# Optimization experiments

Hardware: AMD Instinct MI355X
Metric: run time of the kernel (lower is better)

The kernel has to match this reference:

```python
import jax, jax.numpy as jnp
import numpy as np

L, A, S, D, H = 64, 64, 20, 512, 8
HD = D // H  # head_dim = 64


def _linear(x, W, b):
    # torch nn.Linear: y = x @ W.T + b, W is [out, in]
    return x @ W.T + b


def _mha(q, k, v, mask, Wq, bq, Wk, bk, Wv, bv, Wo, bo):
    # q,k,v: [L, B, D]; mask: [Lq, Lk] additive float mask
    Lq, B, Dm = q.shape
    Lk = k.shape[0]
    scale = 1.0 / np.sqrt(HD)
    qh = _linear(q, Wq, bq).reshape(Lq, B, H, HD) * scale
    kh = _linear(k, Wk, bk).reshape(Lk, B, H, HD)
    vh = _linear(v, Wv, bv).reshape(Lk, B, H, HD)
    scores = jnp.einsum('qbhd,kbhd->bhqk', qh, kh) + mask[None, None, :, :]
    p = jax.nn.softmax(scores, axis=-1)
    o = jnp.einsum('bhqk,kbhd->qbhd', p, vh).reshape(Lq, B, Dm)
    return _linear(o, Wo, bo)


def _forward(query, key, value, attn_mask, Wq, bq, Wk, bk, Wv, bv, Wo, bo,
             Wti, bti, Wtg, btg, seq_mask):
    Lq, Ag, Sm, Dm = query.shape
    Lk = key.shape[0]
    B = Ag * Sm
    # temporal causal mask (torch loop: rows i mask cols > i; built only if seq_mask and Lq==Lk)
    if seq_mask and Lq == Lk:
        tmask = jnp.where(jnp.arange(Lq)[:, None] < jnp.arange(Lk)[None, :],
                          -jnp.inf, 0.0).astype(query.dtype)
    else:
        tmask = jnp.zeros((Lq, Lk), dtype=query.dtype)
    tq = query.reshape(Lq, B, Dm)
    tk = key.reshape(Lk, B, Dm)
    tv = value.reshape(Lk, B, Dm)
    t_attn = _mha(tq, tk, tv, tmask, Wq, bq, Wk, bk, Wv, bv, Wo, bo)
    # GLU-style gated fusion
    t_out = jnp.tanh(_linear(t_attn, Wti, bti)) * jax.nn.sigmoid(_linear(t_attn, Wtg, btg))
    return t_out.reshape(Lq, Ag, Sm, Dm)


def setup_inputs() -> dict:
    key = jax.random.key(0)
    ks = jax.random.split(key, 16)
    sd = 1.0 / np.sqrt(D)
    f32 = jnp.float32
    inp = {
        'query': jax.random.normal(ks[0], (L, A, S, D), f32),
        'key': jax.random.normal(ks[1], (L, A, S, D), f32),
        'value': jax.random.normal(ks[2], (L, A, S, D), f32),
        'attn_mask': jnp.zeros((L, L), f32),
        'Wq': jax.random.normal(ks[3], (D, D), f32) * sd,
        'bq': jnp.zeros((D,), f32),
        'Wk': jax.random.normal(ks[4], (D, D), f32) * sd,
        'bk': jnp.zeros((D,), f32),
        'Wv': jax.random.normal(ks[5], (D, D), f32) * sd,
        'bv': jnp.zeros((D,), f32),
        'Wo': jax.random.normal(ks[6], (D, D), f32) * sd,
        'bo': jnp.zeros((D,), f32),
        'Wti': jax.random.normal(ks[7], (D, D), f32) * sd,
        'bti': jnp.zeros((D,), f32),
        'Wtg': jax.random.normal(ks[8], (D, D), f32) * sd,
        'btg': jnp.zeros((D,), f32),
        'seq_mask': 1,
    }
    return inp


def reference(query, key, value, attn_mask, Wq, bq, Wk, bk, Wv, bv, Wo, bo,
              Wti, bti, Wtg, btg, seq_mask):
    return _forward(query, key, value, attn_mask, Wq, bq, Wk, bk, Wv, bv,
                    Wo, bo, Wti, bti, Wtg, btg, seq_mask)
```

## Files before the change

### kernel.cpp

```cpp
#include <hip/hip_runtime.h>
#include <hip/hip_bf16.h>
#include <math.h>
#include <stdint.h>

typedef __hip_bfloat16 bf16_t;
typedef __bf16 bf16x8 __attribute__((ext_vector_type(8)));
typedef float f32x4 __attribute__((ext_vector_type(4)));

#define MFMA_BF16(a, b, c) __builtin_amdgcn_mfma_f32_16x16x32_bf16((a), (b), (c), 0, 0, 0)

__device__ __forceinline__ uint4 ld8_f32_bf16(const float* p) {
  const float4 x = *(const float4*)p;
  const float4 y = *(const float4*)(p + 4);
  union { bf16_t h[8]; uint4 u; } r;
  r.h[0] = __float2bfloat16(x.x); r.h[1] = __float2bfloat16(x.y);
  r.h[2] = __float2bfloat16(x.z); r.h[3] = __float2bfloat16(x.w);
  r.h[4] = __float2bfloat16(y.x); r.h[5] = __float2bfloat16(y.y);
  r.h[6] = __float2bfloat16(y.z); r.h[7] = __float2bfloat16(y.w);
  return r.u;
}

__global__ __launch_bounds__(256) void gemm_f32(const float* __restrict__ A,
                                                const float* __restrict__ W,
                                                const float* __restrict__ bias,
                                                bf16_t* __restrict__ C, float alpha) {
  const int K = 512, N = 512;
  __shared__ __align__(16) bf16_t As[128 * 32];
  __shared__ __align__(16) bf16_t Bs[128 * 32];
  const int tid = threadIdx.x;
  const int w = tid >> 6, lane = tid & 63;
  const int quad = lane >> 4, l16 = lane & 15;
  const int wm = (w >> 1) * 64, wn = (w & 1) * 64;
  const size_t m0 = (size_t)blockIdx.x * 128;
  const int n0 = blockIdx.y * 128;
  const float* Ab = A + m0 * K;
  const float* Wb = W + (size_t)n0 * K;
  const int r0 = tid >> 2;
  const int c0 = (tid & 3) * 8;
  f32x4 acc[4][4] = {};
  for (int k0 = 0; k0 < K; k0 += 32) {
    const uint4 a0 = ld8_f32_bf16(&Ab[(size_t)r0 * K + k0 + c0]);
    const uint4 a1 = ld8_f32_bf16(&Ab[(size_t)(r0 + 64) * K + k0 + c0]);
    const uint4 b0 = ld8_f32_bf16(&Wb[(size_t)r0 * K + k0 + c0]);
    const uint4 b1 = ld8_f32_bf16(&Wb[(size_t)(r0 + 64) * K + k0 + c0]);
    __syncthreads();
    *(uint4*)&As[r0 * 32 + c0] = a0;
    *(uint4*)&As[(r0 + 64) * 32 + c0] = a1;
    *(uint4*)&Bs[r0 * 32 + c0] = b0;
    *(uint4*)&Bs[(r0 + 64) * 32 + c0] = b1;
    __syncthreads();
    bf16x8 af[4], bfr[4];
#pragma unroll
    for (int i = 0; i < 4; i++)
      af[i] = *(const bf16x8*)&As[(wm + i * 16 + l16) * 32 + quad * 8];
#pragma unroll
    for (int j = 0; j < 4; j++)
      bfr[j] = *(const bf16x8*)&Bs[(wn + j * 16 + l16) * 32 + quad * 8];
#pragma unroll
    for (int i = 0; i < 4; i++)
#pragma unroll
      for (int j = 0; j < 4; j++)
        acc[i][j] = MFMA_BF16(af[i], bfr[j], acc[i][j]);
  }
#pragma unroll
  for (int j = 0; j < 4; j++) {
    const int col = n0 + wn + j * 16 + l16;
    const float bv = bias[col];
#pragma unroll
    for (int i = 0; i < 4; i++) {
      const size_t row = m0 + wm + i * 16 + quad * 4;
#pragma unroll
      for (int v = 0; v < 4; v++) {
        const float x = (acc[i][j][v] + bv) * alpha;
        C[(row + v) * N + col] = __float2bfloat16(x);
      }
    }
  }
}

__global__ __launch_bounds__(256) void gemm_abf16(const bf16_t* __restrict__ A,
                                                  const float* __restrict__ W,
                                                  const float* __restrict__ bias,
                                                  bf16_t* __restrict__ C) {
  const int K = 512, N = 512;
  __shared__ __align__(16) bf16_t As[128 * 32];
  __shared__ __align__(16) bf16_t Bs[128 * 32];
  const int tid = threadIdx.x;
  const int w = tid >> 6, lane = tid & 63;
  const int quad = lane >> 4, l16 = lane & 15;
  const int wm = (w >> 1) * 64, wn = (w & 1) * 64;
  const size_t m0 = (size_t)blockIdx.x * 128;
  const int n0 = blockIdx.y * 128;
  const bf16_t* Ab = A + m0 * K;
  const float* Wb = W + (size_t)n0 * K;
  const int r0 = tid >> 2;
  const int c0 = (tid & 3) * 8;
  f32x4 acc[4][4] = {};
  for (int k0 = 0; k0 < K; k0 += 32) {
    const uint4 a0 = *(const uint4*)&Ab[(size_t)r0 * K + k0 + c0];
    const uint4 a1 = *(const uint4*)&Ab[(size_t)(r0 + 64) * K + k0 + c0];
    const uint4 b0 = ld8_f32_bf16(&Wb[(size_t)r0 * K + k0 + c0]);
    const uint4 b1 = ld8_f32_bf16(&Wb[(size_t)(r0 + 64) * K + k0 + c0]);
    __syncthreads();
    *(uint4*)&As[r0 * 32 + c0] = a0;
    *(uint4*)&As[(r0 + 64) * 32 + c0] = a1;
    *(uint4*)&Bs[r0 * 32 + c0] = b0;
    *(uint4*)&Bs[(r0 + 64) * 32 + c0] = b1;
    __syncthreads();
    bf16x8 af[4], bfr[4];
#pragma unroll
    for (int i = 0; i < 4; i++)
      af[i] = *(const bf16x8*)&As[(wm + i * 16 + l16) * 32 + quad * 8];
#pragma unroll
    for (int j = 0; j < 4; j++)
      bfr[j] = *(const bf16x8*)&Bs[(wn + j * 16 + l16) * 32 + quad * 8];
#pragma unroll
    for (int i = 0; i < 4; i++)
#pragma unroll
      for (int j = 0; j < 4; j++)
        acc[i][j] = MFMA_BF16(af[i], bfr[j], acc[i][j]);
  }
#pragma unroll
  for (int j = 0; j < 4; j++) {
    const int col = n0 + wn + j * 16 + l16;
    const float bv = bias[col];
#pragma unroll
    for (int i = 0; i < 4; i++) {
      const size_t row = m0 + wm + i * 16 + quad * 4;
#pragma unroll
      for (int v = 0; v < 4; v++) {
        const float x = acc[i][j][v] + bv;
        C[(row + v) * N + col] = __float2bfloat16(x);
      }
    }
  }
}

__global__ __launch_bounds__(256) void gemm_gate(const bf16_t* __restrict__ A,
                                                 const float* __restrict__ Wi,
                                                 const float* __restrict__ bi,
                                                 const float* __restrict__ Wg,
                                                 const float* __restrict__ bg,
                                                 float* __restrict__ C) {
  const int K = 512, N = 512;
  __shared__ __align__(16) bf16_t As[128 * 32];
  __shared__ __align__(16) bf16_t Bi[128 * 32];
  __shared__ __align__(16) bf16_t Bg[128 * 32];
  const int tid = threadIdx.x;
  const int w = tid >> 6, lane = tid & 63;
  const int quad = lane >> 4, l16 = lane & 15;
  const int wm = (w >> 1) * 64, wn = (w & 1) * 64;
  const size_t m0 = (size_t)blockIdx.x * 128;
  const int n0 = blockIdx.y * 128;
  const bf16_t* Ab = A + m0 * K;
  const float* Wib = Wi + (size_t)n0 * K;
  const float* Wgb = Wg + (size_t)n0 * K;
  const int r0 = tid >> 2;
  const int c0 = (tid & 3) * 8;
  f32x4 ai[4][4] = {};
  f32x4 ag[4][4] = {};
  for (int k0 = 0; k0 < K; k0 += 32) {
    const uint4 a0 = *(const uint4*)&Ab[(size_t)r0 * K + k0 + c0];
    const uint4 a1 = *(const uint4*)&Ab[(size_t)(r0 + 64) * K + k0 + c0];
    const uint4 i0 = ld8_f32_bf16(&Wib[(size_t)r0 * K + k0 + c0]);
    const uint4 i1 = ld8_f32_bf16(&Wib[(size_t)(r0 + 64) * K + k0 + c0]);
    const uint4 g0 = ld8_f32_bf16(&Wgb[(size_t)r0 * K + k0 + c0]);
    const uint4 g1 = ld8_f32_bf16(&Wgb[(size_t)(r0 + 64) * K + k0 + c0]);
    __syncthreads();
    *(uint4*)&As[r0 * 32 + c0] = a0;
    *(uint4*)&As[(r0 + 64) * 32 + c0] = a1;
    *(uint4*)&Bi[r0 * 32 + c0] = i0;
    *(uint4*)&Bi[(r0 + 64) * 32 + c0] = i1;
    *(uint4*)&Bg[r0 * 32 + c0] = g0;
    *(uint4*)&Bg[(r0 + 64) * 32 + c0] = g1;
    __syncthreads();
    bf16x8 af[4], bif[4], bgf[4];
#pragma unroll
    for (int i = 0; i < 4; i++)
      af[i] = *(const bf16x8*)&As[(wm + i * 16 + l16) * 32 + quad * 8];
#pragma unroll
    for (int j = 0; j < 4; j++) {
      bif[j] = *(const bf16x8*)&Bi[(wn + j * 16 + l16) * 32 + quad * 8];
      bgf[j] = *(const bf16x8*)&Bg[(wn + j * 16 + l16) * 32 + quad * 8];
    }
#pragma unroll
    for (int i = 0; i < 4; i++)
#pragma unroll
      for (int j = 0; j < 4; j++) {
        ai[i][j] = MFMA_BF16(af[i], bif[j], ai[i][j]);
        ag[i][j] = MFMA_BF16(af[i], bgf[j], ag[i][j]);
      }
  }
#pragma unroll
  for (int j = 0; j < 4; j++) {
    const int col = n0 + wn + j * 16 + l16;
    const float bvi = bi[col];
    const float bvg = bg[col];
#pragma unroll
    for (int i = 0; i < 4; i++) {
      const size_t row = m0 + wm + i * 16 + quad * 4;
#pragma unroll
      for (int v = 0; v < 4; v++) {
        const float xi = ai[i][j][v] + bvi;
        const float xg = ag[i][j][v] + bvg;
        C[(row + v) * N + col] = tanhf(xi) * (1.0f / (1.0f + __expf(-xg)));
      }
    }
  }
}

__global__ __launch_bounds__(64) void attn_head(const bf16_t* Qh,
                                                const bf16_t* Kh,
                                                const bf16_t* Vh,
                                                bf16_t* O,
                                                const int* __restrict__ seq_mask) {
  const int B = 1280, D = 512;
  const int b = blockIdx.x >> 3, h = blockIdx.x & 7;
  const int lane = threadIdx.x;
  __shared__ __align__(16) bf16_t Qs[64 * 64];
  __shared__ __align__(16) bf16_t Ks[64 * 64];
  __shared__ __align__(16) bf16_t VT[64 * 64];
  bf16_t* Ps = Qs;
  const size_t cb = (size_t)h * 64;
  for (int idx = lane; idx < 512; idx += 64) {
    const int r = idx >> 3, cg = (idx & 7) << 3;
    const size_t go = (size_t)(r * B + b) * D + cb + cg;
    *(uint4*)&Qs[r * 64 + cg] = *(const uint4*)&Qh[go];
    *(uint4*)&Ks[r * 64 + cg] = *(const uint4*)&Kh[go];
    uint4 vv = *(const uint4*)&Vh[go];
    const bf16_t* vp = (const bf16_t*)&vv;
#pragma unroll
    for (int jj = 0; jj < 8; jj++) VT[(cg + jj) * 64 + r] = vp[jj];
  }
  __syncthreads();
  const int quad = lane >> 4, l16 = lane & 15;
  f32x4 sc[4][4] = {};
#pragma unroll
  for (int ks = 0; ks < 2; ks++) {
    bf16x8 qa[4], kb[4];
#pragma unroll
    for (int i = 0; i < 4; i++)
      qa[i] = *(const bf16x8*)&Qs[(i * 16 + l16) * 64 + ks * 32 + quad * 8];
#pragma unroll
    for (int j = 0; j < 4; j++)
      kb[j] = *(const bf16x8*)&Ks[(j * 16 + l16) * 64 + ks * 32 + quad * 8];
#pragma unroll
    for (int i = 0; i < 4; i++)
#pragma unroll
      for (int j = 0; j < 4; j++)
        sc[i][j] = MFMA_BF16(qa[i], kb[j], sc[i][j]);
  }
  const bool causal = (seq_mask[0] != 0);
  __syncthreads();
#pragma unroll
  for (int i = 0; i < 4; i++) {
#pragma unroll
    for (int v = 0; v < 4; v++) {
      const int r = i * 16 + quad * 4 + v;
      float sv[4];
      float mx = -3e38f;
#pragma unroll
      for (int j = 0; j < 4; j++) {
        const int c = j * 16 + l16;
        float s = sc[i][j][v];
        if (causal && c > r) s = -3e38f;
        sv[j] = s;
        mx = fmaxf(mx, s);
      }
#pragma unroll
      for (int m = 1; m < 16; m <<= 1) mx = fmaxf(mx, __shfl_xor(mx, m, 16));
      float sum = 0.f;
#pragma unroll
      for (int j = 0; j < 4; j++) {
        const float e = (sv[j] <= -1e38f) ? 0.f : __expf(sv[j] - mx);
        sv[j] = e;
        sum += e;
      }
#pragma unroll
      for (int m = 1; m < 16; m <<= 1) sum += __shfl_xor(sum, m, 16);
      const float inv = 1.0f / sum;
#pragma unroll
      for (int j = 0; j < 4; j++)
        Ps[r * 64 + j * 16 + l16] = __float2bfloat16(sv[j] * inv);
    }
  }
  __syncthreads();
  f32x4 oc[4][4] = {};
#pragma unroll
  for (int ks = 0; ks < 2; ks++) {
    bf16x8 pf[4], vf[4];
#pragma unroll
    for (int i = 0; i < 4; i++)
      pf[i] = *(const bf16x8*)&Ps[(i * 16 + l16) * 64 + ks * 32 + quad * 8];
#pragma unroll
    for (int j = 0; j < 4; j++)
      vf[j] = *(const bf16x8*)&VT[(j * 16 + l16) * 64 + ks * 32 + quad * 8];
#pragma unroll
    for (int i = 0; i < 4; i++)
#pragma unroll
      for (int j = 0; j < 4; j++)
        oc[i][j] = MFMA_BF16(pf[i], vf[j], oc[i][j]);
  }
#pragma unroll
  for (int i = 0; i < 4; i++)
#pragma unroll
    for (int j = 0; j < 4; j++) {
      const int c = j * 16 + l16;
#pragma unroll
      for (int v = 0; v < 4; v++) {
        const int r = i * 16 + quad * 4 + v;
        O[(size_t)(r * B + b) * D + cb + c] = __float2bfloat16(oc[i][j][v]);
      }
    }
}

extern "C" void kernel_launch(void* const* d_in, const int* in_sizes, int n_in,
                              void* d_out, int out_size, void* d_ws, size_t ws_size,
                              hipStream_t stream) {
  const float* query = (const float*)d_in[0];
  const float* key_ = (const float*)d_in[1];
  const float* value = (const float*)d_in[2];
  const float* Wq = (const float*)d_in[4];
  const float* bq = (const float*)d_in[5];
  const float* Wk = (const float*)d_in[6];
  const float* bk = (const float*)d_in[7];
  const float* Wv = (const float*)d_in[8];
  const float* bv = (const float*)d_in[9];
  const float* Wo = (const float*)d_in[10];
  const float* bo = (const float*)d_in[11];
  const float* Wti = (const float*)d_in[12];
  const float* bti = (const float*)d_in[13];
  const float* Wtg = (const float*)d_in[14];
  const float* btg = (const float*)d_in[15];
  const int* seq_mask = (const int*)d_in[16];
  float* out = (float*)d_out;

  const size_t M = 81920;
  const size_t buf = M * 512;
  bf16_t* Qh = (bf16_t*)d_ws;
  bf16_t* Kh = Qh + buf;
  bf16_t* Vh = Kh + buf;
  bf16_t* Ob = Qh;
  bf16_t* Ta = Kh;

  dim3 gg(640, 4), gb(256);
  hipLaunchKernelGGL(gemm_f32, gg, gb, 0, stream, query, Wq, bq, Qh, 0.125f);
  hipLaunchKernelGGL(gemm_f32, gg, gb, 0, stream, key_, Wk, bk, Kh, 1.0f);
  hipLaunchKernelGGL(gemm_f32, gg, gb, 0, stream, value, Wv, bv, Vh, 1.0f);
  hipLaunchKernelGGL(attn_head, dim3(10240), dim3(64), 0, stream, Qh, Kh, Vh, Ob, seq_mask);
  hipLaunchKernelGGL(gemm_abf16, gg, gb, 0, stream, Ob, Wo, bo, Ta);
  hipLaunchKernelGGL(gemm_gate, gg, gb, 0, stream, Ta, Wti, bti, Wtg, btg, out);
}
```

Baseline: 1.311 ms.

## Pre-convert weights to bf16 and stage GEMM tiles via direct global-to-LDS loads

A new kernel converts all six fp32 weight matrices to bf16 once per call into extra workspace. This removes the per-block fp32-to-bf16 conversion and halves weight read traffic in every GEMM tile. The bf16 operand tiles are now copied with global_load_lds straight into shared memory, skipping the register round-trip. The fp32-input projection GEMM also prefetches the next A tile into registers before the MFMA loop. The cost is one extra small launch and more workspace, and correctness relies on the LDS DMA lane layout and on completion before the barrier.

```diff
diff --git a/kernel.cpp b/kernel.cpp
--- a/kernel.cpp
+++ b/kernel.cpp
@@ -20,10 +20,43 @@
   return r.u;
 }
 
-__global__ __launch_bounds__(256) void gemm_f32(const float* __restrict__ A,
-                                                const float* __restrict__ W,
-                                                const float* __restrict__ bias,
-                                                bf16_t* __restrict__ C, float alpha) {
+__device__ __forceinline__ uint4 pack8_bf16(const float4 x, const float4 y) {
+  union { bf16_t h[8]; uint4 u; } r;
+  r.h[0] = __float2bfloat16(x.x); r.h[1] = __float2bfloat16(x.y);
+  r.h[2] = __float2bfloat16(x.z); r.h[3] = __float2bfloat16(x.w);
+  r.h[4] = __float2bfloat16(y.x); r.h[5] = __float2bfloat16(y.y);
+  r.h[6] = __float2bfloat16(y.z); r.h[7] = __float2bfloat16(y.w);
+  return r.u;
+}
+
+__device__ __forceinline__ void gload16(const bf16_t* g, bf16_t* lds) {
+  __builtin_amdgcn_global_load_lds(
+      (const __attribute__((address_space(1))) void*)g,
+      (__attribute__((address_space(3))) void*)lds, 16, 0, 0);
+}
+
+__global__ __launch_bounds__(256) void cvt_w6(const float* __restrict__ W0,
+                                              const float* __restrict__ W1,
+                                              const float* __restrict__ W2,
+                                              const float* __restrict__ W3,
+                                              const float* __restrict__ W4,
+                                              const float* __restrict__ W5,
+                                              bf16_t* __restrict__ dst) {
+  const int m = blockIdx.y;
+  const float* src = W0;
+  if (m == 1) src = W1;
+  else if (m == 2) src = W2;
+  else if (m == 3) src = W3;
+  else if (m == 4) src = W4;
+  else if (m == 5) src = W5;
+  const size_t i = ((size_t)blockIdx.x * 256 + threadIdx.x) * 8;
+  *(uint4*)&dst[(size_t)m * 262144 + i] = ld8_f32_bf16(&src[i]);
+}
+
+__global__ __launch_bounds__(256) void gemm_aw(const float* __restrict__ A,
+                                               const bf16_t* __restrict__ W,
+                                               const float* __restrict__ bias,
+                                               bf16_t* __restrict__ C, float alpha) {
   const int K = 512, N = 512;
   __shared__ __align__(16) bf16_t As[128 * 32];
   __shared__ __align__(16) bf16_t Bs[128 * 32];
@@ -34,20 +67,22 @@
   const size_t m0 = (size_t)blockIdx.x * 128;
   const int n0 = blockIdx.y * 128;
   const float* Ab = A + m0 * K;
-  const float* Wb = W + (size_t)n0 * K;
+  const bf16_t* Wb = W + (size_t)n0 * K;
   const int r0 = tid >> 2;
   const int c0 = (tid & 3) * 8;
   f32x4 acc[4][4] = {};
+  float4 pa0 = *(const float4*)&Ab[(size_t)r0 * K + c0];
+  float4 pa1 = *(const float4*)&Ab[(size_t)r0 * K + c0 + 4];
+  float4 pa2 = *(const float4*)&Ab[(size_t)(r0 + 64) * K + c0];
+  float4 pa3 = *(const float4*)&Ab[(size_t)(r0 + 64) * K + c0 + 4];
   for (int k0 = 0; k0 < K; k0 += 32) {
-    const uint4 a0 = ld8_f32_bf16(&Ab[(size_t)r0 * K + k0 + c0]);
-    const uint4 a1 = ld8_f32_bf16(&Ab[(size_t)(r0 + 64) * K + k0 + c0]);
-    const uint4 b0 = ld8_f32_bf16(&Wb[(size_t)r0 * K + k0 + c0]);
-    const uint4 b1 = ld8_f32_bf16(&Wb[(size_t)(r0 + 64) * K + k0 + c0]);
-    __syncthreads();
+    const uint4 a0 = pack8_bf16(pa0, pa1);
+    const uint4 a1 = pack8_bf16(pa2, pa3);
+    __syncthreads();
+    gload16(&Wb[(size_t)r0 * K + k0 + c0], &Bs[w * 512]);
+    gload16(&Wb[(size_t)(r0 + 64) * K + k0 + c0], &Bs[2048 + w * 512]);
     *(uint4*)&As[r0 * 32 + c0] = a0;
     *(uint4*)&As[(r0 + 64) * 32 + c0] = a1;
-    *(uint4*)&Bs[r0 * 32 + c0] = b0;
-    *(uint4*)&Bs[(r0 + 64) * 32 + c0] = b1;
     __syncthreads();
     bf16x8 af[4], bfr[4];
 #pragma unroll
@@ -56,6 +91,12 @@
 #pragma unroll
     for (int j = 0; j < 4; j++)
       bfr[j] = *(const bf16x8*)&Bs[(wn + j * 16 + l16) * 32 + quad * 8];
+    if (k0 + 32 < K) {
+      pa0 = *(const float4*)&Ab[(size_t)r0 * K + k0 + 32 + c0];
+      pa1 = *(const float4*)&Ab[(size_t)r0 * K + k0 + 32 + c0 + 4];
+      pa2 = *(const float4*)&Ab[(size_t)(r0 + 64) * K + k0 + 32 + c0];
+      pa3 = *(const float4*)&Ab[(size_t)(r0 + 64) * K + k0 + 32 + c0 + 4];
+    }
 #pragma unroll
     for (int i = 0; i < 4; i++)
 #pragma unroll
@@ -78,10 +119,10 @@
   }
 }
 
-__global__ __launch_bounds__(256) void gemm_abf16(const bf16_t* __restrict__ A,
-                                                  const float* __restrict__ W,
-                                                  const float* __restrict__ bias,
-                                                  bf16_t* __restrict__ C) {
+__global__ __launch_bounds__(256) void gemm_bb(const bf16_t* __restrict__ A,
+                                               const bf16_t* __restrict__ W,
+                                               const float* __restrict__ bias,
+                                               bf16_t* __restrict__ C) {
   const int K = 512, N = 512;
   __shared__ __align__(16) bf16_t As[128 * 32];
   __shared__ __align__(16) bf16_t Bs[128 * 32];
@@ -92,20 +133,16 @@
   const size_t m0 = (size_t)blockIdx.x * 128;
   const int n0 = blockIdx.y * 128;
   const bf16_t* Ab = A + m0 * K;
-  const float* Wb = W + (size_t)n0 * K;
+  const bf16_t* Wb = W + (size_t)n0 * K;
   const int r0 = tid >> 2;
   const int c0 = (tid & 3) * 8;
   f32x4 acc[4][4] = {};
   for (int k0 = 0; k0 < K; k0 += 32) {
-    const uint4 a0 = *(const uint4*)&Ab[(size_t)r0 * K + k0 + c0];
-    const uint4 a1 = *(const uint4*)&Ab[(size_t)(r0 + 64) * K + k0 + c0];
-    const uint4 b0 = ld8_f32_bf16(&Wb[(size_t)r0 * K + k0 + c0]);
-    const uint4 b1 = ld8_f32_bf16(&Wb[(size_t)(r0 + 64) * K + k0 + c0]);
-    __syncthreads();
-    *(uint4*)&As[r0 * 32 + c0] = a0;
-    *(uint4*)&As[(r0 + 64) * 32 + c0] = a1;
-    *(uint4*)&Bs[r0 * 32 + c0] = b0;
-    *(uint4*)&Bs[(r0 + 64) * 32 + c0] = b1;
+    __syncthreads();
+    gload16(&Ab[(size_t)r0 * K + k0 + c0], &As[w * 512]);
+    gload16(&Ab[(size_t)(r0 + 64) * K + k0 + c0], &As[2048 + w * 512]);
+    gload16(&Wb[(size_t)r0 * K + k0 + c0], &Bs[w * 512]);
+    gload16(&Wb[(size_t)(r0 + 64) * K + k0 + c0], &Bs[2048 + w * 512]);
     __syncthreads();
     bf16x8 af[4], bfr[4];
 #pragma unroll
@@ -136,12 +173,12 @@
   }
 }
 
-__global__ __launch_bounds__(256) void gemm_gate(const bf16_t* __restrict__ A,
-                                                 const float* __restrict__ Wi,
-                                                 const float* __restrict__ bi,
-                                                 const float* __restrict__ Wg,
-                                                 const float* __restrict__ bg,
-                                                 float* __restrict__ C) {
+__global__ __launch_bounds__(256) void gemm_gate2(const bf16_t* __restrict__ A,
+                                                  const bf16_t* __restrict__ Wi,
+                                                  const float* __restrict__ bi,
+                                                  const bf16_t* __restrict__ Wg,
+                                                  const float* __restrict__ bg,
+                                                  float* __restrict__ C) {
   const int K = 512, N = 512;
   __shared__ __align__(16) bf16_t As[128 * 32];
   __shared__ __align__(16) bf16_t Bi[128 * 32];
@@ -153,26 +190,20 @@
   const size_t m0 = (size_t)blockIdx.x * 128;
   const int n0 = blockIdx.y * 128;
   const bf16_t* Ab = A + m0 * K;
-  const float* Wib = Wi + (size_t)n0 * K;
-  const float* Wgb = Wg + (size_t)n0 * K;
+  const bf16_t* Wib = Wi + (size_t)n0 * K;
+  const bf16_t* Wgb = Wg + (size_t)n0 * K;
   const int r0 = tid >> 2;
   const int c0 = (tid & 3) * 8;
   f32x4 ai[4][4] = {};
   f32x4 ag[4][4] = {};
   for (int k0 = 0; k0 < K; k0 += 32) {
-    const uint4 a0 = *(const uint4*)&Ab[(size_t)r0 * K + k0 + c0];
-    const uint4 a1 = *(const uint4*)&Ab[(size_t)(r0 + 64) * K + k0 + c0];
-    const uint4 i0 = ld8_f32_bf16(&Wib[(size_t)r0 * K + k0 + c0]);
-    const uint4 i1 = ld8_f32_bf16(&Wib[(size_t)(r0 + 64) * K + k0 + c0]);
-    const uint4 g0 = ld8_f32_bf16(&Wgb[(size_t)r0 * K + k0 + c0]);
-    const uint4 g1 = ld8_f32_bf16(&Wgb[(size_t)(r0 + 64) * K + k0 + c0]);
-    __syncthreads();
-    *(uint4*)&As[r0 * 32 + c0] = a0;
-    *(uint4*)&As[(r0 + 64) * 32 + c0] = a1;
-    *(uint4*)&Bi[r0 * 32 + c0] = i0;
-    *(uint4*)&Bi[(r0 + 64) * 32 + c0] = i1;
-    *(uint4*)&Bg[r0 * 32 + c0] = g0;
-    *(uint4*)&Bg[(r0 + 64) * 32 + c0] = g1;
+    __syncthreads();
+    gload16(&Ab[(size_t)r0 * K + k0 + c0], &As[w * 512]);
+    gload16(&Ab[(size_t)(r0 + 64) * K + k0 + c0], &As[2048 + w * 512]);
+    gload16(&Wib[(size_t)r0 * K + k0 + c0], &Bi[w * 512]);
+    gload16(&Wib[(size_t)(r0 + 64) * K + k0 + c0], &Bi[2048 + w * 512]);
+    gload16(&Wgb[(size_t)r0 * K + k0 + c0], &Bg[w * 512]);
+    gload16(&Wgb[(size_t)(r0 + 64) * K + k0 + c0], &Bg[2048 + w * 512]);
     __syncthreads();
     bf16x8 af[4], bif[4], bgf[4];
 #pragma unroll
@@ -337,17 +368,26 @@
 
   const size_t M = 81920;
   const size_t buf = M * 512;
+  const size_t wsz = 512 * 512;
   bf16_t* Qh = (bf16_t*)d_ws;
   bf16_t* Kh = Qh + buf;
   bf16_t* Vh = Kh + buf;
+  bf16_t* Wbase = Vh + buf;
+  bf16_t* Wqb = Wbase + 0 * wsz;
+  bf16_t* Wkb = Wbase + 1 * wsz;
+  bf16_t* Wvb = Wbase + 2 * wsz;
+  bf16_t* Wob = Wbase + 3 * wsz;
+  bf16_t* Wtib = Wbase + 4 * wsz;
+  bf16_t* Wtgb = Wbase + 5 * wsz;
   bf16_t* Ob = Qh;
   bf16_t* Ta = Kh;
 
   dim3 gg(640, 4), gb(256);
-  hipLaunchKernelGGL(gemm_f32, gg, gb, 0, stream, query, Wq, bq, Qh, 0.125f);
-  hipLaunchKernelGGL(gemm_f32, gg, gb, 0, stream, key_, Wk, bk, Kh, 1.0f);
-  hipLaunchKernelGGL(gemm_f32, gg, gb, 0, stream, value, Wv, bv, Vh, 1.0f);
+  hipLaunchKernelGGL(cvt_w6, dim3(128, 6), gb, 0, stream, Wq, Wk, Wv, Wo, Wti, Wtg, Wbase);
+  hipLaunchKernelGGL(gemm_aw, gg, gb, 0, stream, query, Wqb, bq, Qh, 0.125f);
+  hipLaunchKernelGGL(gemm_aw, gg, gb, 0, stream, key_, Wkb, bk, Kh, 1.0f);
+  hipLaunchKernelGGL(gemm_aw, gg, gb, 0, stream, value, Wvb, bv, Vh, 1.0f);
   hipLaunchKernelGGL(attn_head, dim3(10240), dim3(64), 0, stream, Qh, Kh, Vh, Ob, seq_mask);
-  hipLaunchKernelGGL(gemm_abf16, gg, gb, 0, stream, Ob, Wo, bo, Ta);
-  hipLaunchKernelGGL(gemm_gate, gg, gb, 0, stream, Ta, Wti, bti, Wtg, btg, out);
-}
+  hipLaunchKernelGGL(gemm_bb, gg, gb, 0, stream, Ob, Wob, bo, Ta);
+  hipLaunchKernelGGL(gemm_gate2, gg, gb, 0, stream, Ta, Wtib, bti, Wtgb, btg, out);
+}
```

New measurement: 1.225 ms. 1.07x faster.
